# Kernel optimization log

Measured on AMD Instinct MI355X. Metric: run time of the kernel, lower is better.

## Reference

```python
import jax, jax.numpy as jnp
import numpy as np

HEADS = 16
HEAD_DIM = 64  # hidden_size 1024 / 16 heads
NUM_TOKENS = 4
IP_SCALE = 1.0
LN_EPS = 1e-5


def setup_inputs() -> dict:
    key = jax.random.key(0)
    ks = jax.random.split(key, 12)
    B, Lq, D, Dc = 8, 4096, 1024, 768
    Lenc = 77 + NUM_TOKENS
    s = lambda fan: 1.0 / np.sqrt(fan)
    return {
        "hidden_states": jax.random.normal(ks[0], (B, Lq, D), jnp.float32),
        "encoder_hidden_states": jax.random.normal(ks[1], (B, Lenc, Dc), jnp.float32),
        "Wq": jax.random.normal(ks[2], (D, D), jnp.float32) * s(D),
        "Wk": jax.random.normal(ks[3], (D, Dc), jnp.float32) * s(Dc),
        "Wv": jax.random.normal(ks[4], (D, Dc), jnp.float32) * s(Dc),
        "Wk_ip": jax.random.normal(ks[5], (D, Dc), jnp.float32) * s(Dc),
        "Wv_ip": jax.random.normal(ks[6], (D, Dc), jnp.float32) * s(Dc),
        "Wo": jax.random.normal(ks[7], (D, D), jnp.float32) * s(D),
        "bo": jnp.zeros((D,), jnp.float32),
        "ln_w": jnp.ones((Dc,), jnp.float32),
        "ln_b": jnp.zeros((Dc,), jnp.float32),
    }


def _layernorm(x, w, b):
    mu = jnp.mean(x, axis=-1, keepdims=True)
    var = jnp.var(x, axis=-1, keepdims=True)
    return (x - mu) * jax.lax.rsqrt(var + LN_EPS) * w + b


def _heads(x):
    B, L, D = x.shape
    return x.reshape(B, L, HEADS, HEAD_DIM)


def _attend(q, k, v):
    # q: [B,Lq,H,Dh], k/v: [B,Lk,H,Dh]
    scale = 1.0 / np.sqrt(HEAD_DIM)
    scores = jnp.einsum("bqhd,bkhd->bhqk", q, k) * scale
    probs = jax.nn.softmax(scores, axis=-1)
    return jnp.einsum("bhqk,bkhd->bqhd", probs, v)


def reference(hidden_states, encoder_hidden_states, Wq, Wk, Wv, Wk_ip, Wv_ip, Wo, bo, ln_w, ln_b):
    B, Lq, D = hidden_states.shape
    end_pos = encoder_hidden_states.shape[1] - NUM_TOKENS
    text = encoder_hidden_states[:, :end_pos, :]
    ip = encoder_hidden_states[:, end_pos:, :]
    text = _layernorm(text, ln_w, ln_b)  # attn.norm_cross

    q = _heads(hidden_states @ Wq.T)
    k = _heads(text @ Wk.T)
    v = _heads(text @ Wv.T)
    base = _attend(q, k, v)  # [B,Lq,H,Dh]

    ip_k = _heads(ip @ Wk_ip.T)
    ip_v = _heads(ip @ Wv_ip.T)
    ip_out = _attend(q, ip_k, ip_v)

    out = (base + IP_SCALE * ip_out).reshape(B, Lq, D)
    return out @ Wo.T + bo
```

## Files before the change

kernel.cpp:

```cpp
#include <hip/hip_runtime.h>
#include <hip/hip_bf16.h>
#include <stdint.h>


typedef __attribute__((ext_vector_type(8))) short short8;
typedef __attribute__((ext_vector_type(4))) float f32x4;
typedef __attribute__((ext_vector_type(8))) float float8_t;
typedef __attribute__((ext_vector_type(8))) __bf16 bf16x8;
typedef __attribute__((ext_vector_type(4))) __bf16 bf16x4;

__device__ __forceinline__ ushort f2b(float f) {
  __bf16 h = (__bf16)f;
  return __builtin_bit_cast(ushort, h);
}

#define GLD16(gp, lp) \
  __builtin_amdgcn_global_load_lds((const __attribute__((address_space(1))) uint32_t*)(gp), \
                                   (__attribute__((address_space(3))) uint32_t*)(lp), 16, 0, 0)

#define FENCE_SCHED() __builtin_amdgcn_sched_barrier(0)

struct CvtArgs {
  const float* src[6];
  ushort* dst[6];
  int n4[6];
};

__global__ __launch_bounds__(256) void k_prep(CvtArgs a,
                                              const float* __restrict__ enc,
                                              const float* __restrict__ lnw,
                                              const float* __restrict__ lnb,
                                              ushort* __restrict__ xn,
                                              const float* __restrict__ hs,
                                              ushort* __restrict__ hs_bf) {
  int seg = blockIdx.y;
  if (seg < 6) {
    int i = blockIdx.x * blockDim.x + threadIdx.x;
    if (i >= a.n4[seg]) return;
    float4 v = reinterpret_cast<const float4*>(a.src[seg])[i];
    bf16x4 h;
    h[0] = (__bf16)v.x; h[1] = (__bf16)v.y; h[2] = (__bf16)v.z; h[3] = (__bf16)v.w;
    reinterpret_cast<ushort4*>(a.dst[seg])[i] = __builtin_bit_cast(ushort4, h);
    return;
  }
  if (seg == 7) {
    const int n4 = 8388608;
    for (int i = blockIdx.x * 256 + threadIdx.x; i < n4; i += 1024 * 256) {
      float4 v = reinterpret_cast<const float4*>(hs)[i];
      bf16x4 h;
      h[0] = (__bf16)v.x; h[1] = (__bf16)v.y; h[2] = (__bf16)v.z; h[3] = (__bf16)v.w;
      reinterpret_cast<ushort4*>(hs_bf)[i] = __builtin_bit_cast(ushort4, h);
    }
    return;
  }
  if (blockIdx.x >= 768) return;
  const int Dc = 768;
  int tok = blockIdx.x % 96, b = blockIdx.x / 96, t = threadIdx.x;
  ushort* out = xn + ((size_t)b * 96 + tok) * Dc;
  bool padrow = (tok >= 84) || (tok >= 77 && tok < 80);
  if (padrow) { out[t] = 0; out[t + 256] = 0; out[t + 512] = 0; return; }
  const float* src = (tok < 77) ? enc + ((size_t)b * 81 + tok) * Dc
                                : enc + ((size_t)b * 81 + 77 + (tok - 80)) * Dc;
  float x0 = src[t], x1 = src[t + 256], x2 = src[t + 512];
  if (tok >= 80) { out[t] = f2b(x0); out[t + 256] = f2b(x1); out[t + 512] = f2b(x2); return; }
  float s = x0 + x1 + x2, q = x0 * x0 + x1 * x1 + x2 * x2;
  for (int m = 32; m; m >>= 1) { s += __shfl_xor(s, m, 64); q += __shfl_xor(q, m, 64); }
  __shared__ float rs[4], rq[4];
  int w = t >> 6;
  if ((t & 63) == 0) { rs[w] = s; rq[w] = q; }
  __syncthreads();
  s = rs[0] + rs[1] + rs[2] + rs[3];
  q = rq[0] + rq[1] + rq[2] + rq[3];
  float mean = s * (1.0f / 768.0f);
  float var = q * (1.0f / 768.0f) - mean * mean;
  float rstd = rsqrtf(var + 1e-5f);
  out[t]       = f2b((x0 - mean) * rstd * lnw[t]       + lnb[t]);
  out[t + 256] = f2b((x1 - mean) * rstd * lnw[t + 256] + lnb[t + 256]);
  out[t + 512] = f2b((x2 - mean) * rstd * lnw[t + 512] + lnb[t + 512]);
}

__global__ __launch_bounds__(256) void k_kv(const ushort* __restrict__ xn,
                                            const ushort* __restrict__ wk,
                                            const ushort* __restrict__ wkip,
                                            const ushort* __restrict__ wv,
                                            const ushort* __restrict__ wvip,
                                            ushort* __restrict__ kall,
                                            ushort* __restrict__ vtall) {
  int mode = blockIdx.z;
  const ushort* wb   = mode ? wv   : wk;
  const ushort* wipb = mode ? wvip : wkip;
  ushort* out        = mode ? vtall : kall;
  int n0 = blockIdx.x * 64, b = blockIdx.y;
  int t = threadIdx.x, w = t >> 6, l = t & 63, lo = l & 15, hi = l >> 4;
  __shared__ alignas(16) ushort Xs[96 * 32];
  __shared__ alignas(16) ushort Ws[64 * 32];
  __shared__ alignas(16) ushort Wip[64 * 32];
  f32x4 acc[6];
  f32x4 zf = {0.f, 0.f, 0.f, 0.f};
  for (int i = 0; i < 6; i++) acc[i] = zf;
  const ushort* xb = xn + (size_t)b * 96 * 768;
  for (int k0 = 0; k0 < 768; k0 += 32) {
    __syncthreads();
    for (int i = t; i < 96 * 16; i += 256) {
      int row = i >> 4, p = i & 15;
      reinterpret_cast<uint32_t*>(Xs)[i] =
          *reinterpret_cast<const uint32_t*>(xb + row * 768 + k0 + p * 2);
    }
    for (int i = t; i < 64 * 16; i += 256) {
      int row = i >> 4, p = i & 15;
      reinterpret_cast<uint32_t*>(Ws)[i] =
          *reinterpret_cast<const uint32_t*>(wb + (size_t)(n0 + row) * 768 + k0 + p * 2);
      reinterpret_cast<uint32_t*>(Wip)[i] =
          *reinterpret_cast<const uint32_t*>(wipb + (size_t)(n0 + row) * 768 + k0 + p * 2);
    }
    __syncthreads();
    short8 a[6], bb, bip;
    for (int mi = 0; mi < 6; mi++)
      a[mi] = *reinterpret_cast<const short8*>(Xs + (mi * 16 + lo) * 32 + hi * 8);
    bb  = *reinterpret_cast<const short8*>(Ws  + (w * 16 + lo) * 32 + hi * 8);
    bip = *reinterpret_cast<const short8*>(Wip + (w * 16 + lo) * 32 + hi * 8);
    for (int mi = 0; mi < 5; mi++)
      acc[mi] = __builtin_amdgcn_mfma_f32_16x16x32_bf16(a[mi], bb, acc[mi], 0, 0, 0);
    acc[5] = __builtin_amdgcn_mfma_f32_16x16x32_bf16(a[5], bip, acc[5], 0, 0, 0);
  }
  for (int mi = 0; mi < 6; mi++) {
    int col = n0 + w * 16 + lo;
    int h = col >> 6, dd = col & 63;
    for (int j = 0; j < 4; j++) {
      int tok = mi * 16 + hi * 4 + j;
      ushort v = f2b(acc[mi][j]);
      if (mode == 0) out[(((size_t)b * 16 + h) * 96 + tok) * 64 + dd] = v;
      else           out[(((size_t)b * 16 + h) * 64 + dd) * 96 + tok] = v;
    }
  }
}

__global__ __launch_bounds__(512, 2) void k_qg8(const ushort* __restrict__ A,
                                                const ushort* __restrict__ Bw,
                                                const ushort* __restrict__ Kall,
                                                const ushort* __restrict__ Vt,
                                                ushort* __restrict__ attnO) {
  const int K = 1024, NT = 16;
  int wg = blockIdx.x;
  int nid = (wg & 7) * 64 + (wg >> 3);
  int m0 = (nid >> 2) * 256, n0 = (nid & 3) * 256;
  int t = threadIdx.x, wid = t >> 6, l = t & 63, lo = l & 15, hi = l >> 4;
  int wr = wid >> 2, wc = wid & 3;
  __shared__ alignas(16) ushort SMEM[81920];
  ushort* ASb = SMEM;
  ushort* BSb = SMEM + 32768;
  f32x4 acc[8][4];
  f32x4 zf = {0.f, 0.f, 0.f, 0.f};
#pragma unroll
  for (int i = 0; i < 8; i++)
#pragma unroll
    for (int j = 0; j < 4; j++) acc[i][j] = zf;
  int tr = t >> 3, tc = t & 7;
  int tcs = tc ^ (tr & 7);
  const ushort* gA = A  + (size_t)(m0 + tr) * K + tcs * 8;
  const ushort* gB = Bw + (size_t)(n0 + tr) * K + tcs * 8;

#define STG_A(kt_, s_, b_) GLD16(gA + (size_t)(s_) * 64 * K + (kt_) * 64, &ASb[(b_) * 16384 + (s_) * 4096 + wid * 512])
#define STG_B(kt_, s_, b_) GLD16(gB + (size_t)(s_) * 64 * K + (kt_) * 64, &BSb[(b_) * 16384 + (s_) * 4096 + wid * 512])

  STG_A(0, 0, 0); STG_A(0, 1, 0); STG_A(0, 2, 0); STG_A(0, 3, 0);
  STG_B(0, 0, 0); STG_B(0, 1, 0); STG_B(0, 2, 0); STG_B(0, 3, 0);
  STG_B(1, 0, 1); STG_B(1, 1, 1); STG_B(1, 2, 1); STG_B(1, 3, 1);
  STG_A(1, 0, 1); STG_A(1, 1, 1);
  asm volatile("s_waitcnt vmcnt(6)" ::: "memory");
  __builtin_amdgcn_s_barrier();
  FENCE_SCHED();

  const int swz = (lo & 7) << 3;
  short8 af[4][2], af2[4][2], b01[2][2], b23[2][2];

  for (int kt = 0; kt < NT; kt++) {
    int cur = kt & 1, nxt = cur ^ 1;
    const ushort* sA = &ASb[cur * 16384];
    const ushort* sB = &BSb[cur * 16384];
#pragma unroll
    for (int q = 0; q < 4; q++)
#pragma unroll
      for (int kk = 0; kk < 2; kk++)
        af[q][kk] = *reinterpret_cast<const short8*>(
            sA + (wr * 128 + q * 16 + lo) * 64 + ((hi * 8 + kk * 32) ^ swz));
#pragma unroll
    for (int n = 0; n < 2; n++)
#pragma unroll
      for (int kk = 0; kk < 2; kk++) {
        b01[n][kk] = *reinterpret_cast<const short8*>(
            sB + (wc * 64 + n * 16 + lo) * 64 + ((hi * 8 + kk * 32) ^ swz));
        b23[n][kk] = *reinterpret_cast<const short8*>(
            sB + (wc * 64 + (2 + n) * 16 + lo) * 64 + ((hi * 8 + kk * 32) ^ swz));
      }
    if (kt + 1 < NT) { STG_A(kt + 1, 2, nxt); STG_A(kt + 1, 3, nxt); }
    __builtin_amdgcn_s_barrier();
    FENCE_SCHED();
    __builtin_amdgcn_s_setprio(1);
#pragma unroll
    for (int q = 0; q < 4; q++)
#pragma unroll
      for (int n = 0; n < 2; n++)
#pragma unroll
        for (int kk = 0; kk < 2; kk++) {
          acc[q][n]     = __builtin_amdgcn_mfma_f32_16x16x32_bf16(af[q][kk], b01[n][kk], acc[q][n], 0, 0, 0);
          acc[q][2 + n] = __builtin_amdgcn_mfma_f32_16x16x32_bf16(af[q][kk], b23[n][kk], acc[q][2 + n], 0, 0, 0);
        }
    __builtin_amdgcn_s_setprio(0);
    __builtin_amdgcn_s_barrier();
    FENCE_SCHED();
#pragma unroll
    for (int q = 0; q < 4; q++)
#pragma unroll
      for (int kk = 0; kk < 2; kk++)
        af2[q][kk] = *reinterpret_cast<const short8*>(
            sA + (wr * 128 + (4 + q) * 16 + lo) * 64 + ((hi * 8 + kk * 32) ^ swz));
    if (kt + 2 < NT) { STG_B(kt + 2, 0, cur); STG_B(kt + 2, 1, cur); }
    __builtin_amdgcn_s_barrier();
    FENCE_SCHED();
    __builtin_amdgcn_s_setprio(1);
#pragma unroll
    for (int q = 0; q < 4; q++)
#pragma unroll
      for (int n = 0; n < 2; n++)
#pragma unroll
        for (int kk = 0; kk < 2; kk++)
          acc[4 + q][2 + n] = __builtin_amdgcn_mfma_f32_16x16x32_bf16(af2[q][kk], b23[n][kk], acc[4 + q][2 + n], 0, 0, 0);
    __builtin_amdgcn_s_setprio(0);
    __builtin_amdgcn_s_barrier();
    FENCE_SCHED();
    if (kt + 2 < NT) {
      STG_B(kt + 2, 2, cur); STG_B(kt + 2, 3, cur);
      STG_A(kt + 2, 0, cur); STG_A(kt + 2, 1, cur);
      asm volatile("s_waitcnt vmcnt(6)" ::: "memory");
    } else {
      asm volatile("s_waitcnt vmcnt(0)" ::: "memory");
    }
    __builtin_amdgcn_s_barrier();
    FENCE_SCHED();
    __builtin_amdgcn_s_setprio(1);
#pragma unroll
    for (int q = 0; q < 4; q++)
#pragma unroll
      for (int n = 0; n < 2; n++)
#pragma unroll
        for (int kk = 0; kk < 2; kk++)
          acc[4 + q][n] = __builtin_amdgcn_mfma_f32_16x16x32_bf16(af2[q][kk], b01[n][kk], acc[4 + q][n], 0, 0, 0);
    __builtin_amdgcn_s_setprio(0);
    __builtin_amdgcn_s_barrier();
    FENCE_SCHED();
  }
#undef STG_A
#undef STG_B

  __syncthreads();
  ushort* ep = SMEM + wid * 8192;
#pragma unroll
  for (int mi = 0; mi < 8; mi++)
#pragma unroll
    for (int n = 0; n < 4; n++)
#pragma unroll
      for (int j = 0; j < 4; j++) {
        int row_l = mi * 16 + hi * 4 + j;
        int col = n * 16 + lo;
        ep[row_l * 64 + (((col >> 3) ^ (row_l & 7)) << 3) + (col & 7)] = f2b(acc[mi][n][j]);
      }
  ushort* PS = SMEM + 65536 + wid * 2048;
  int b = m0 >> 12;
  int h = (n0 >> 6) + wc;
  const ushort* Kb = Kall + (size_t)(b * 16 + h) * 96 * 64;
  const ushort* Vb = Vt + (size_t)(b * 16 + h) * 64 * 96;
  short8 kf[6][2], vf[3][4];
#pragma unroll
  for (int ni = 0; ni < 6; ni++)
#pragma unroll
    for (int ks = 0; ks < 2; ks++)
      kf[ni][ks] = *reinterpret_cast<const short8*>(Kb + (ni * 16 + lo) * 64 + ks * 32 + hi * 8);
#pragma unroll
  for (int kk = 0; kk < 3; kk++)
#pragma unroll
    for (int dn = 0; dn < 4; dn++)
      vf[kk][dn] = *reinterpret_cast<const short8*>(Vb + (dn * 16 + lo) * 96 + kk * 32 + hi * 8);
  const float SC = 0.125f * 1.44269504088896340736f;

  short8 qf[2];
  f32x4 s[6];
#define QK_LOAD(mi_) do { \
    _Pragma("unroll") \
    for (int ks = 0; ks < 2; ks++) \
      qf[ks] = *reinterpret_cast<const short8*>( \
          &ep[((mi_) * 16 + lo) * 64 + (((ks * 4 + hi) ^ (lo & 7)) << 3)]); \
  } while (0)
#define QK_MFMA() do { \
    _Pragma("unroll") \
    for (int ni = 0; ni < 6; ni++) { \
      s[ni] = zf; \
      _Pragma("unroll") \
      for (int ks = 0; ks < 2; ks++) \
        s[ni] = __builtin_amdgcn_mfma_f32_16x16x32_bf16(qf[ks], kf[ni][ks], s[ni], 0, 0, 0); \
    } } while (0)

  QK_LOAD(0); QK_MFMA();
  for (int mi = 0; mi < 8; mi++) {
    float rb4[4];
#pragma unroll
    for (int j = 0; j < 4; j++) {
      float pb[5];
      float sb = 0.f;
#pragma unroll
      for (int ni = 0; ni < 5; ni++) {
        int c = ni * 16 + lo;
        float p = (c < 77) ? exp2f(s[ni][j] * SC) : 0.f;
        pb[ni] = p; sb += p;
      }
      sb += __shfl_xor(sb, 1, 64); sb += __shfl_xor(sb, 2, 64);
      sb += __shfl_xor(sb, 4, 64); sb += __shfl_xor(sb, 8, 64);
      rb4[j] = __builtin_amdgcn_rcpf(sb);
      bool val = lo < 4;
      float pi = val ? exp2f(s[5][j] * SC) : 0.f;
      float si = pi;
      si += __shfl_xor(si, 1, 64); si += __shfl_xor(si, 2, 64);
      ushort* pr = &PS[(hi * 4 + j) * 104];
#pragma unroll
      for (int ni = 0; ni < 5; ni++) pr[ni * 16 + lo] = f2b(pb[ni]);
      pr[80 + lo] = f2b(val ? pi * (sb * __builtin_amdgcn_rcpf(si)) : 0.f);
    }
    if (mi < 7) { QK_LOAD(mi + 1); QK_MFMA(); }
    f32x4 o[4];
#pragma unroll
    for (int dn = 0; dn < 4; dn++) o[dn] = zf;
#pragma unroll
    for (int kk = 0; kk < 3; kk++) {
      short8 pf = *reinterpret_cast<const short8*>(&PS[lo * 104 + kk * 32 + hi * 8]);
#pragma unroll
      for (int dn = 0; dn < 4; dn++)
        o[dn] = __builtin_amdgcn_mfma_f32_16x16x32_bf16(pf, vf[kk][dn], o[dn], 0, 0, 0);
    }
#pragma unroll
    for (int dn = 0; dn < 4; dn++)
#pragma unroll
      for (int j = 0; j < 4; j++) {
        int row_l = hi * 4 + j;
        int col = dn * 16 + lo;
        PS[row_l * 64 + (((col >> 3) ^ (row_l & 7)) << 3) + (col & 7)] = f2b(o[dn][j] * rb4[j]);
      }
    int gr0 = m0 + wr * 128 + mi * 16;
#pragma unroll
    for (int it = 0; it < 2; it++) {
      int row_o = it * 8 + (l >> 3), c8 = l & 7;
      short8 v = *reinterpret_cast<const short8*>(
          &PS[row_o * 64 + ((c8 ^ (row_o & 7)) << 3)]);
      *reinterpret_cast<short8*>(&attnO[(size_t)(gr0 + row_o) * 1024 + h * 64 + c8 * 8]) = v;
    }
  }
#undef QK_LOAD
#undef QK_MFMA
}

__global__ __launch_bounds__(512, 2) void k_og8(const ushort* __restrict__ A,
                                                const ushort* __restrict__ Bw,
                                                const float* __restrict__ bias,
                                                float* __restrict__ C) {
  const int K = 1024, NT = 16;
  int wg = blockIdx.x;
  int nid = (wg & 7) * 64 + (wg >> 3);
  int m0 = (nid >> 2) * 256, n0 = (nid & 3) * 256;
  int t = threadIdx.x, wid = t >> 6, l = t & 63, lo = l & 15, hi = l >> 4;
  int wr = wid >> 2, wc = wid & 3;
  __shared__ alignas(16) ushort AS[2][256 * 64];
  __shared__ alignas(16) ushort BS[2][256 * 64];
  f32x4 acc[8][4];
  f32x4 zf = {0.f, 0.f, 0.f, 0.f};
#pragma unroll
  for (int i = 0; i < 8; i++)
#pragma unroll
    for (int j = 0; j < 4; j++) acc[i][j] = zf;
  int tr = t >> 3, tc = t & 7;
  int tcs = tc ^ (tr & 7);
  const ushort* gA = A  + (size_t)(m0 + tr) * K + tcs * 8;
  const ushort* gB = Bw + (size_t)(n0 + tr) * K + tcs * 8;

#define STG_A(kt_, s_, b_) GLD16(gA + (size_t)(s_) * 64 * K + (kt_) * 64, &AS[b_][(s_) * 4096 + wid * 512])
#define STG_B(kt_, s_, b_) GLD16(gB + (size_t)(s_) * 64 * K + (kt_) * 64, &BS[b_][(s_) * 4096 + wid * 512])

  STG_A(0, 0, 0); STG_A(0, 1, 0); STG_A(0, 2, 0); STG_A(0, 3, 0);
  STG_B(0, 0, 0); STG_B(0, 1, 0); STG_B(0, 2, 0); STG_B(0, 3, 0);
  STG_B(1, 0, 1); STG_B(1, 1, 1); STG_B(1, 2, 1); STG_B(1, 3, 1);
  STG_A(1, 0, 1); STG_A(1, 1, 1);
  asm volatile("s_waitcnt vmcnt(6)" ::: "memory");
  __builtin_amdgcn_s_barrier();
  FENCE_SCHED();

  const int swz = (lo & 7) << 3;
  short8 af[4][2], af2[4][2], b01[2][2], b23[2][2];

  for (int kt = 0; kt < NT; kt++) {
    int cur = kt & 1, nxt = cur ^ 1;
    const ushort* sA = &AS[cur][0];
    const ushort* sB = &BS[cur][0];
#pragma unroll
    for (int q = 0; q < 4; q++)
#pragma unroll
      for (int kk = 0; kk < 2; kk++)
        af[q][kk] = *reinterpret_cast<const short8*>(
            sA + (wr * 128 + q * 16 + lo) * 64 + ((hi * 8 + kk * 32) ^ swz));
#pragma unroll
    for (int n = 0; n < 2; n++)
#pragma unroll
      for (int kk = 0; kk < 2; kk++) {
        b01[n][kk] = *reinterpret_cast<const short8*>(
            sB + (wc * 64 + n * 16 + lo) * 64 + ((hi * 8 + kk * 32) ^ swz));
        b23[n][kk] = *reinterpret_cast<const short8*>(
            sB + (wc * 64 + (2 + n) * 16 + lo) * 64 + ((hi * 8 + kk * 32) ^ swz));
      }
    if (kt + 1 < NT) { STG_A(kt + 1, 2, nxt); STG_A(kt + 1, 3, nxt); }
    __builtin_amdgcn_s_barrier();
    FENCE_SCHED();
    __builtin_amdgcn_s_setprio(1);
#pragma unroll
    for (int q = 0; q < 4; q++)
#pragma unroll
      for (int n = 0; n < 2; n++)
#pragma unroll
        for (int kk = 0; kk < 2; kk++) {
          acc[q][n]     = __builtin_amdgcn_mfma_f32_16x16x32_bf16(af[q][kk], b01[n][kk], acc[q][n], 0, 0, 0);
          acc[q][2 + n] = __builtin_amdgcn_mfma_f32_16x16x32_bf16(af[q][kk], b23[n][kk], acc[q][2 + n], 0, 0, 0);
        }
    __builtin_amdgcn_s_setprio(0);
    __builtin_amdgcn_s_barrier();
    FENCE_SCHED();
#pragma unroll
    for (int q = 0; q < 4; q++)
#pragma unroll
      for (int kk = 0; kk < 2; kk++)
        af2[q][kk] = *reinterpret_cast<const short8*>(
            sA + (wr * 128 + (4 + q) * 16 + lo) * 64 + ((hi * 8 + kk * 32) ^ swz));
    if (kt + 2 < NT) { STG_B(kt + 2, 0, cur); STG_B(kt + 2, 1, cur); }
    __builtin_amdgcn_s_barrier();
    FENCE_SCHED();
    __builtin_amdgcn_s_setprio(1);
#pragma unroll
    for (int q = 0; q < 4; q++)
#pragma unroll
      for (int n = 0; n < 2; n++)
#pragma unroll
        for (int kk = 0; kk < 2; kk++)
          acc[4 + q][2 + n] = __builtin_amdgcn_mfma_f32_16x16x32_bf16(af2[q][kk], b23[n][kk], acc[4 + q][2 + n], 0, 0, 0);
    __builtin_amdgcn_s_setprio(0);
    __builtin_amdgcn_s_barrier();
    FENCE_SCHED();
    if (kt + 2 < NT) {
      STG_B(kt + 2, 2, cur); STG_B(kt + 2, 3, cur);
      STG_A(kt + 2, 0, cur); STG_A(kt + 2, 1, cur);
      asm volatile("s_waitcnt vmcnt(6)" ::: "memory");
    } else {
      asm volatile("s_waitcnt vmcnt(0)" ::: "memory");
    }
    __builtin_amdgcn_s_barrier();
    FENCE_SCHED();
    __builtin_amdgcn_s_setprio(1);
#pragma unroll
    for (int q = 0; q < 4; q++)
#pragma unroll
      for (int n = 0; n < 2; n++)
#pragma unroll
        for (int kk = 0; kk < 2; kk++)
          acc[4 + q][n] = __builtin_amdgcn_mfma_f32_16x16x32_bf16(af2[q][kk], b01[n][kk], acc[4 + q][n], 0, 0, 0);
    __builtin_amdgcn_s_setprio(0);
    __builtin_amdgcn_s_barrier();
    FENCE_SCHED();
  }
#pragma unroll
  for (int n = 0; n < 4; n++) {
    int c = n0 + wc * 64 + n * 16 + lo;
    float bv = bias[c];
#pragma unroll
    for (int mi = 0; mi < 8; mi++)
#pragma unroll
      for (int j = 0; j < 4; j++) {
        int r = m0 + wr * 128 + mi * 16 + hi * 4 + j;
        C[(size_t)r * 1024 + c] = acc[mi][n][j] + bv;
      }
  }
#undef STG_A
#undef STG_B
}

extern "C" void kernel_launch(void* const* d_in, const int* in_sizes, int n_in,
                              void* d_out, int out_size, void* d_ws, size_t ws_size,
                              hipStream_t stream) {
  const float* hs   = (const float*)d_in[0];
  const float* enc  = (const float*)d_in[1];
  const float* Wq   = (const float*)d_in[2];
  const float* Wk   = (const float*)d_in[3];
  const float* Wv   = (const float*)d_in[4];
  const float* Wkip = (const float*)d_in[5];
  const float* Wvip = (const float*)d_in[6];
  const float* Wo   = (const float*)d_in[7];
  const float* bo   = (const float*)d_in[8];
  const float* lnw  = (const float*)d_in[9];
  const float* lnb  = (const float*)d_in[10];
  float* out = (float*)d_out;
  ushort* hs_bf = (ushort*)d_out + (size_t)32768 * 1024;

  ushort* p = (ushort*)d_ws;
  ushort* attn    = p; p += (size_t)32768 * 1024;
  ushort* wq_bf   = p; p += (size_t)1024 * 1024;
  ushort* wo_bf   = p; p += (size_t)1024 * 1024;
  ushort* wk_bf   = p; p += (size_t)1024 * 768;
  ushort* wkip_bf = p; p += (size_t)1024 * 768;
  ushort* wv_bf   = p; p += (size_t)1024 * 768;
  ushort* wvip_bf = p; p += (size_t)1024 * 768;
  ushort* xn      = p; p += (size_t)8 * 96 * 768;
  ushort* kall    = p; p += (size_t)8 * 16 * 96 * 64;
  ushort* vtall   = p; p += (size_t)8 * 16 * 96 * 64;

  CvtArgs ca;
  ca.src[0] = Wq;   ca.dst[0] = wq_bf;   ca.n4[0] = 262144;
  ca.src[1] = Wo;   ca.dst[1] = wo_bf;   ca.n4[1] = 262144;
  ca.src[2] = Wk;   ca.dst[2] = wk_bf;   ca.n4[2] = 196608;
  ca.src[3] = Wkip; ca.dst[3] = wkip_bf; ca.n4[3] = 196608;
  ca.src[4] = Wv;   ca.dst[4] = wv_bf;   ca.n4[4] = 196608;
  ca.src[5] = Wvip; ca.dst[5] = wvip_bf; ca.n4[5] = 196608;
  k_prep<<<dim3(1024, 8), 256, 0, stream>>>(ca, enc, lnw, lnb, xn, hs, hs_bf);
  k_kv<<<dim3(16, 8, 2), 256, 0, stream>>>(xn, wk_bf, wkip_bf, wv_bf, wvip_bf, kall, vtall);
  k_qg8<<<512, 512, 0, stream>>>(hs_bf, wq_bf, kall, vtall, attn);
  k_og8<<<512, 512, 0, stream>>>(attn, wo_bf, bo, out);
}
```

Measured before the change: 289.6 us.

## Fuse LayerNorm and K/V projection into the prep kernel, drop k_kv launch

The separate K/V projection kernel is folded into the prep kernel as an extra grid segment. Each block recomputes LayerNorm statistics for its batch's text rows and converts encoder rows and fp32 K/V weights to bf16 while loading them into shared memory. This removes a kernel launch, the bf16 weight and xn intermediates, and a pass over global memory. In exchange, every block redundantly recomputes row stats and weight conversions, uses uncoalesced scalar fp32 loads, and the KV work now sits alongside the large hs conversion in the same grid.

```diff
diff --git a/kernel.cpp b/kernel.cpp
--- a/kernel.cpp
+++ b/kernel.cpp
@@ -20,32 +20,41 @@
 
 #define FENCE_SCHED() __builtin_amdgcn_sched_barrier(0)
 
-struct CvtArgs {
-  const float* src[6];
-  ushort* dst[6];
-  int n4[6];
-};
-
-__global__ __launch_bounds__(256) void k_prep(CvtArgs a,
+__global__ __launch_bounds__(256) void k_prep(const float* __restrict__ Wq,
+                                              const float* __restrict__ Wo,
+                                              ushort* __restrict__ wq_bf,
+                                              ushort* __restrict__ wo_bf,
+                                              const float* __restrict__ hs,
+                                              ushort* __restrict__ hs_bf,
                                               const float* __restrict__ enc,
                                               const float* __restrict__ lnw,
                                               const float* __restrict__ lnb,
-                                              ushort* __restrict__ xn,
-                                              const float* __restrict__ hs,
-                                              ushort* __restrict__ hs_bf) {
+                                              const float* __restrict__ Wk,
+                                              const float* __restrict__ Wkip,
+                                              const float* __restrict__ Wv,
+                                              const float* __restrict__ Wvip,
+                                              ushort* __restrict__ kall,
+                                              ushort* __restrict__ vtall) {
+  __shared__ alignas(16) ushort Xs[96 * 32];
+  __shared__ alignas(16) ushort Ws[64 * 32];
+  __shared__ alignas(16) ushort Wip[64 * 32];
+  __shared__ float stat_m[96], stat_r[96];
+
   int seg = blockIdx.y;
-  if (seg < 6) {
-    int i = blockIdx.x * blockDim.x + threadIdx.x;
-    if (i >= a.n4[seg]) return;
-    float4 v = reinterpret_cast<const float4*>(a.src[seg])[i];
+  int t = threadIdx.x;
+  if (seg == 0 || seg == 1) {
+    const float* src = seg ? Wo : Wq;
+    ushort* dst = seg ? wo_bf : wq_bf;
+    int i = blockIdx.x * 256 + t;
+    float4 v = reinterpret_cast<const float4*>(src)[i];
     bf16x4 h;
     h[0] = (__bf16)v.x; h[1] = (__bf16)v.y; h[2] = (__bf16)v.z; h[3] = (__bf16)v.w;
-    reinterpret_cast<ushort4*>(a.dst[seg])[i] = __builtin_bit_cast(ushort4, h);
+    reinterpret_cast<ushort4*>(dst)[i] = __builtin_bit_cast(ushort4, h);
     return;
   }
-  if (seg == 7) {
+  if (seg == 2) {
     const int n4 = 8388608;
-    for (int i = blockIdx.x * 256 + threadIdx.x; i < n4; i += 1024 * 256) {
+    for (int i = blockIdx.x * 256 + t; i < n4; i += 1024 * 256) {
       float4 v = reinterpret_cast<const float4*>(hs)[i];
       bf16x4 h;
       h[0] = (__bf16)v.x; h[1] = (__bf16)v.y; h[2] = (__bf16)v.z; h[3] = (__bf16)v.w;
@@ -53,65 +62,61 @@
     }
     return;
   }
-  if (blockIdx.x >= 768) return;
-  const int Dc = 768;
-  int tok = blockIdx.x % 96, b = blockIdx.x / 96, t = threadIdx.x;
-  ushort* out = xn + ((size_t)b * 96 + tok) * Dc;
-  bool padrow = (tok >= 84) || (tok >= 77 && tok < 80);
-  if (padrow) { out[t] = 0; out[t + 256] = 0; out[t + 512] = 0; return; }
-  const float* src = (tok < 77) ? enc + ((size_t)b * 81 + tok) * Dc
-                                : enc + ((size_t)b * 81 + 77 + (tok - 80)) * Dc;
-  float x0 = src[t], x1 = src[t + 256], x2 = src[t + 512];
-  if (tok >= 80) { out[t] = f2b(x0); out[t + 256] = f2b(x1); out[t + 512] = f2b(x2); return; }
-  float s = x0 + x1 + x2, q = x0 * x0 + x1 * x1 + x2 * x2;
-  for (int m = 32; m; m >>= 1) { s += __shfl_xor(s, m, 64); q += __shfl_xor(q, m, 64); }
-  __shared__ float rs[4], rq[4];
-  int w = t >> 6;
-  if ((t & 63) == 0) { rs[w] = s; rq[w] = q; }
+  if (blockIdx.x >= 256) return;
+  int bid = blockIdx.x;
+  int mode = bid >> 7;
+  int b    = (bid >> 4) & 7;
+  int n0   = (bid & 15) * 64;
+  int w = t >> 6, l = t & 63, lo = l & 15, hi = l >> 4;
+  const float* wsel   = mode ? Wv   : Wk;
+  const float* wipsel = mode ? Wvip : Wkip;
+  ushort* outp        = mode ? vtall : kall;
+
+  for (int r = w; r < 77; r += 4) {
+    const float* row = enc + ((size_t)b * 81 + r) * 768;
+    float sum = 0.f, sq = 0.f;
+    for (int c = l; c < 768; c += 64) {
+      float x = row[c];
+      sum += x; sq += x * x;
+    }
+    for (int m = 32; m; m >>= 1) { sum += __shfl_xor(sum, m, 64); sq += __shfl_xor(sq, m, 64); }
+    if (l == 0) {
+      float mean = sum * (1.0f / 768.0f);
+      float var = sq * (1.0f / 768.0f) - mean * mean;
+      stat_m[r] = mean;
+      stat_r[r] = rsqrtf(var + 1e-5f);
+    }
+  }
   __syncthreads();
-  s = rs[0] + rs[1] + rs[2] + rs[3];
-  q = rq[0] + rq[1] + rq[2] + rq[3];
-  float mean = s * (1.0f / 768.0f);
-  float var = q * (1.0f / 768.0f) - mean * mean;
-  float rstd = rsqrtf(var + 1e-5f);
-  out[t]       = f2b((x0 - mean) * rstd * lnw[t]       + lnb[t]);
-  out[t + 256] = f2b((x1 - mean) * rstd * lnw[t + 256] + lnb[t + 256]);
-  out[t + 512] = f2b((x2 - mean) * rstd * lnw[t + 512] + lnb[t + 512]);
-}
-
-__global__ __launch_bounds__(256) void k_kv(const ushort* __restrict__ xn,
-                                            const ushort* __restrict__ wk,
-                                            const ushort* __restrict__ wkip,
-                                            const ushort* __restrict__ wv,
-                                            const ushort* __restrict__ wvip,
-                                            ushort* __restrict__ kall,
-                                            ushort* __restrict__ vtall) {
-  int mode = blockIdx.z;
-  const ushort* wb   = mode ? wv   : wk;
-  const ushort* wipb = mode ? wvip : wkip;
-  ushort* out        = mode ? vtall : kall;
-  int n0 = blockIdx.x * 64, b = blockIdx.y;
-  int t = threadIdx.x, w = t >> 6, l = t & 63, lo = l & 15, hi = l >> 4;
-  __shared__ alignas(16) ushort Xs[96 * 32];
-  __shared__ alignas(16) ushort Ws[64 * 32];
-  __shared__ alignas(16) ushort Wip[64 * 32];
+
   f32x4 acc[6];
   f32x4 zf = {0.f, 0.f, 0.f, 0.f};
   for (int i = 0; i < 6; i++) acc[i] = zf;
-  const ushort* xb = xn + (size_t)b * 96 * 768;
+
   for (int k0 = 0; k0 < 768; k0 += 32) {
     __syncthreads();
     for (int i = t; i < 96 * 16; i += 256) {
-      int row = i >> 4, p = i & 15;
-      reinterpret_cast<uint32_t*>(Xs)[i] =
-          *reinterpret_cast<const uint32_t*>(xb + row * 768 + k0 + p * 2);
+      int row = i >> 4, p = i & 15, c = k0 + p * 2;
+      ushort u0 = 0, u1 = 0;
+      if (row < 77) {
+        const float* base = enc + ((size_t)b * 81 + row) * 768;
+        float mn = stat_m[row], rs = stat_r[row];
+        u0 = f2b((base[c]     - mn) * rs * lnw[c]     + lnb[c]);
+        u1 = f2b((base[c + 1] - mn) * rs * lnw[c + 1] + lnb[c + 1]);
+      } else if (row >= 80 && row < 84) {
+        const float* base = enc + ((size_t)b * 81 + 77 + (row - 80)) * 768;
+        u0 = f2b(base[c]); u1 = f2b(base[c + 1]);
+      }
+      reinterpret_cast<uint32_t*>(Xs)[i] = (uint32_t)u0 | ((uint32_t)u1 << 16);
     }
     for (int i = t; i < 64 * 16; i += 256) {
-      int row = i >> 4, p = i & 15;
+      int row = i >> 4, p = i & 15, c = k0 + p * 2;
+      const float* wsrc  = wsel   + (size_t)(n0 + row) * 768;
+      const float* wisrc = wipsel + (size_t)(n0 + row) * 768;
       reinterpret_cast<uint32_t*>(Ws)[i] =
-          *reinterpret_cast<const uint32_t*>(wb + (size_t)(n0 + row) * 768 + k0 + p * 2);
+          (uint32_t)f2b(wsrc[c]) | ((uint32_t)f2b(wsrc[c + 1]) << 16);
       reinterpret_cast<uint32_t*>(Wip)[i] =
-          *reinterpret_cast<const uint32_t*>(wipb + (size_t)(n0 + row) * 768 + k0 + p * 2);
+          (uint32_t)f2b(wisrc[c]) | ((uint32_t)f2b(wisrc[c + 1]) << 16);
     }
     __syncthreads();
     short8 a[6], bb, bip;
@@ -129,8 +134,8 @@
     for (int j = 0; j < 4; j++) {
       int tok = mi * 16 + hi * 4 + j;
       ushort v = f2b(acc[mi][j]);
-      if (mode == 0) out[(((size_t)b * 16 + h) * 96 + tok) * 64 + dd] = v;
-      else           out[(((size_t)b * 16 + h) * 64 + dd) * 96 + tok] = v;
+      if (mode == 0) outp[(((size_t)b * 16 + h) * 96 + tok) * 64 + dd] = v;
+      else           outp[(((size_t)b * 16 + h) * 64 + dd) * 96 + tok] = v;
     }
   }
 }
@@ -504,26 +509,15 @@
   ushort* hs_bf = (ushort*)d_out + (size_t)32768 * 1024;
 
   ushort* p = (ushort*)d_ws;
-  ushort* attn    = p; p += (size_t)32768 * 1024;
-  ushort* wq_bf   = p; p += (size_t)1024 * 1024;
-  ushort* wo_bf   = p; p += (size_t)1024 * 1024;
-  ushort* wk_bf   = p; p += (size_t)1024 * 768;
-  ushort* wkip_bf = p; p += (size_t)1024 * 768;
-  ushort* wv_bf   = p; p += (size_t)1024 * 768;
-  ushort* wvip_bf = p; p += (size_t)1024 * 768;
-  ushort* xn      = p; p += (size_t)8 * 96 * 768;
-  ushort* kall    = p; p += (size_t)8 * 16 * 96 * 64;
-  ushort* vtall   = p; p += (size_t)8 * 16 * 96 * 64;
-
-  CvtArgs ca;
-  ca.src[0] = Wq;   ca.dst[0] = wq_bf;   ca.n4[0] = 262144;
-  ca.src[1] = Wo;   ca.dst[1] = wo_bf;   ca.n4[1] = 262144;
-  ca.src[2] = Wk;   ca.dst[2] = wk_bf;   ca.n4[2] = 196608;
-  ca.src[3] = Wkip; ca.dst[3] = wkip_bf; ca.n4[3] = 196608;
-  ca.src[4] = Wv;   ca.dst[4] = wv_bf;   ca.n4[4] = 196608;
-  ca.src[5] = Wvip; ca.dst[5] = wvip_bf; ca.n4[5] = 196608;
-  k_prep<<<dim3(1024, 8), 256, 0, stream>>>(ca, enc, lnw, lnb, xn, hs, hs_bf);
-  k_kv<<<dim3(16, 8, 2), 256, 0, stream>>>(xn, wk_bf, wkip_bf, wv_bf, wvip_bf, kall, vtall);
+  ushort* attn  = p; p += (size_t)32768 * 1024;
+  ushort* wq_bf = p; p += (size_t)1024 * 1024;
+  ushort* wo_bf = p; p += (size_t)1024 * 1024;
+  ushort* kall  = p; p += (size_t)8 * 16 * 96 * 64;
+  ushort* vtall = p; p += (size_t)8 * 16 * 96 * 64;
+
+  k_prep<<<dim3(1024, 4), 256, 0, stream>>>(Wq, Wo, wq_bf, wo_bf, hs, hs_bf,
+                                            enc, lnw, lnb, Wk, Wkip, Wv, Wvip,
+                                            kall, vtall);
   k_qg8<<<512, 512, 0, stream>>>(hs_bf, wq_bf, kall, vtall, attn);
   k_og8<<<512, 512, 0, stream>>>(attn, wo_bf, bo, out);
 }
```

Result: slower. 379.2 us (+30.9%).
